# Performance work log

Hardware: AMD Instinct MI355X
Metric: run time of the kernel (lower is better)

The kernel has to match this reference:

```python
import jax, jax.numpy as jnp
import numpy as np

N, E = 50000, 800000
IN_CH, N_HID, OUT_CH = 128, 256, 128
DROPOUT_P = 0.5


def gcn_conv(x, src, dst, ew, W, b, num_nodes):
    # PyG GCNConv with edge_weight: symmetric normalization with self-loops.
    loop = jnp.arange(num_nodes)
    s = jnp.concatenate([src, loop])
    d = jnp.concatenate([dst, loop])
    w = jnp.concatenate([ew, jnp.ones((num_nodes,), ew.dtype)])
    deg = jax.ops.segment_sum(w, d, num_segments=num_nodes)  # [N]
    dinv = jnp.where(deg > 0, jax.lax.rsqrt(deg), 0.0)
    norm = dinv[s] * w * dinv[d]                             # [E+N]
    h = x @ W                                                # [N, out]
    msg = h[s] * norm[:, None]                               # [E+N, out]
    out = jax.ops.segment_sum(msg, d, num_segments=num_nodes)
    return out + b


def setup_inputs() -> dict:
    key = jax.random.key(0)
    ks = jax.random.split(key, 8)
    x = jax.random.normal(ks[0], (N, IN_CH), dtype=jnp.float32)
    edge_index = jax.random.randint(ks[1], (2, E), 0, N, dtype=jnp.int64)
    weight = jax.random.uniform(ks[2], (E,), dtype=jnp.float32)
    # GCNConv params (glorot weights, zero bias)
    s1 = (6.0 / (IN_CH + N_HID)) ** 0.5
    s2 = (6.0 / (N_HID + OUT_CH)) ** 0.5
    W1 = jax.random.uniform(ks[3], (IN_CH, N_HID), jnp.float32, -s1, s1)
    b1 = jnp.zeros((N_HID,), jnp.float32)
    W2 = jax.random.uniform(ks[4], (N_HID, OUT_CH), jnp.float32, -s2, s2)
    b2 = jnp.zeros((OUT_CH,), jnp.float32)
    return {"x": x, "edge_index": edge_index, "weight": weight,
            "W1": W1, "b1": b1, "W2": W2, "b2": b2}


def reference(x, edge_index, weight, W1, b1, W2, b2):
    src, dst = edge_index[0], edge_index[1]
    h = jax.nn.relu(gcn_conv(x, src, dst, weight, W1, b1, N))
    # F.dropout(x, p) with training=True (torch default); fixed key for determinism
    keep = jax.random.bernoulli(jax.random.key(42), 1.0 - DROPOUT_P, h.shape)
    h = jnp.where(keep, h / (1.0 - DROPOUT_P), 0.0)
    return gcn_conv(h, src, dst, weight, W2, b2, N)
```

## Files before the change

kernel.cpp:

```cpp
#include <hip/hip_runtime.h>
#include <hip/hip_bf16.h>
#include <cstdint>

#define INCH 128
#define NHID 256
#define OUTCH 128
#define CAP 64

typedef unsigned short u16;
typedef unsigned long long u64;
typedef __attribute__((ext_vector_type(8))) short s8v;
typedef __attribute__((ext_vector_type(4))) float f4v;

__device__ __forceinline__ u16 tob(float a) {
    unsigned u = __float_as_uint(a);
    return (u16)((u + 0x7fffu + ((u >> 16) & 1u)) >> 16);
}

__device__ __forceinline__ void bsplit(float a, u16& hi, u16& lo) {
    unsigned u = __float_as_uint(a);
    unsigned r = (u + 0x7fffu + ((u >> 16) & 1u)) >> 16;
    hi = (u16)r;
    float res = a - __uint_as_float(r << 16);
    lo = tob(res);
}

__device__ __forceinline__ unsigned rotl32(unsigned x, int d) {
    return (x << d) | (x >> (32 - d));
}

__device__ __forceinline__ void threefry2x32(unsigned k0, unsigned k1,
                                             unsigned x0, unsigned x1,
                                             unsigned& o0, unsigned& o1) {
    unsigned ks2 = k0 ^ k1 ^ 0x1BD11BDAu;
#define TF_R(r) { x0 += x1; x1 = rotl32(x1, (r)); x1 ^= x0; }
    x0 += k0; x1 += k1;
    TF_R(13) TF_R(15) TF_R(26) TF_R(6)
    x0 += k1; x1 += ks2 + 1u;
    TF_R(17) TF_R(29) TF_R(16) TF_R(24)
    x0 += ks2; x1 += k0 + 2u;
    TF_R(13) TF_R(15) TF_R(26) TF_R(6)
    x0 += k0; x1 += k1 + 3u;
    TF_R(17) TF_R(29) TF_R(16) TF_R(24)
    x0 += k1; x1 += ks2 + 4u;
    TF_R(13) TF_R(15) TF_R(26) TF_R(6)
    x0 += ks2; x1 += k0 + 5u;
#undef TF_R
    o0 = x0; o1 = x1;
}

__global__ __launch_bounds__(256) void k_mask(unsigned* __restrict__ mask, int nwords) {
    int i = blockIdx.x * 256 + threadIdx.x;
    if (i >= nwords) return;
    unsigned base = (unsigned)i * 32u;
    unsigned m = 0;
#pragma unroll
    for (int b = 0; b < 32; ++b) {
        unsigned o0, o1;
        threefry2x32(0u, 42u, 0u, base + (unsigned)b, o0, o1);
        m |= ((((o0 ^ o1) >> 31) ^ 1u) & 1u) << b;
    }
    mask[i] = m;
}

__global__ void k_zero(int* cnt, int N) {
    int i = blockIdx.x * blockDim.x + threadIdx.x;
    if (i < N) cnt[i] = 0;
}

__global__ void k_fill(const int* __restrict__ src, const int* __restrict__ dst,
                       const float* __restrict__ w, int* cnt,
                       unsigned* __restrict__ buck, int E) {
    int e = blockIdx.x * blockDim.x + threadIdx.x;
    if (e < E) {
        int d = dst[e];
        int pos = atomicAdd(&cnt[d], 1);
        if (pos < CAP)
            buck[(size_t)d * CAP + pos] = ((unsigned)tob(w[e]) << 16) | (unsigned)src[e];
    }
}

__global__ __launch_bounds__(256) void k_deg(const unsigned* __restrict__ buck,
                                             const int* __restrict__ cnt,
                                             float* __restrict__ dinv, int N) {
    int node = blockIdx.x * 8 + (threadIdx.x >> 5);
    int l = threadIdx.x & 31;
    if (node >= N) return;
    int c = min(cnt[node], CAP);
    float s = 0.f;
    for (int p = l; p < c; p += 32)
        s += __uint_as_float(buck[(size_t)node * CAP + p] & 0xffff0000u);
#pragma unroll
    for (int o = 16; o > 0; o >>= 1) s += __shfl_xor(s, o, 32);
    if (l == 0) dinv[node] = rsqrtf(1.f + s);
}

__global__ __launch_bounds__(256) void k_norm(unsigned* __restrict__ buck,
                                              const int* __restrict__ cnt,
                                              const float* __restrict__ dinv, int N) {
    int node = blockIdx.x * 8 + (threadIdx.x >> 5);
    int l = threadIdx.x & 31;
    if (node >= N) return;
    int c = min(cnt[node], CAP);
    float dd = dinv[node];
    for (int p = l; p < c; p += 32) {
        unsigned u = buck[(size_t)node * CAP + p];
        unsigned s = u & 0xffffu;
        float wv = __uint_as_float(u & 0xffff0000u);
        float v = dinv[s] * wv * dd;
        buck[(size_t)node * CAP + p] = ((unsigned)tob(v) << 16) | s;
    }
}

__global__ void conv_wt(const float* __restrict__ W, u16* __restrict__ Wh,
                        u16* __restrict__ Wl, int K, int N) {
    int i = blockIdx.x * 256 + threadIdx.x;
    if (i >= K * N) return;
    int k = i / N, n = i % N;
    u16 hi, lo;
    bsplit(W[i], hi, lo);
    Wh[(size_t)n * K + k] = hi;
    Wl[(size_t)n * K + k] = lo;
}

__global__ __launch_bounds__(256) void k_tobf16(const float4* __restrict__ in,
                                                uint4* __restrict__ outb, int n8) {
    int i = blockIdx.x * 256 + threadIdx.x;
    if (i >= n8) return;
    float4 a = in[i * 2], b = in[i * 2 + 1];
    uint4 o;
    o.x = (unsigned)tob(a.x) | ((unsigned)tob(a.y) << 16);
    o.y = (unsigned)tob(a.z) | ((unsigned)tob(a.w) << 16);
    o.z = (unsigned)tob(b.x) | ((unsigned)tob(b.y) << 16);
    o.w = (unsigned)tob(b.z) | ((unsigned)tob(b.w) << 16);
    outb[i] = o;
}

template <int BM, int BN, int MODE>
__global__ __launch_bounds__(256) void gemm_mfma(
    const u16* __restrict__ Ah, const u16* __restrict__ Al,
    const u16* __restrict__ Bh, const u16* __restrict__ Bl,
    const float* __restrict__ bias, const unsigned* __restrict__ mask,
    const float* __restrict__ dinv,
    u16* __restrict__ Ch, u16* __restrict__ Cl,
    u16* __restrict__ Cb, float* __restrict__ Sp,
    int M, int Ntot, int K) {
    constexpr int WN = BN / 2;
    constexpr int MFRAG = BM / 32;
    constexpr int NFRAG = WN / 16;
    __shared__ u16 Alh[BM][40], All[BM][40];
    __shared__ u16 Blh[BN][40], Bll[BN][40];

    const int tid = threadIdx.x;
    const int lane = tid & 63;
    const int w = tid >> 6;
    const int wm = (w >> 1) * (BM / 2);
    const int wn = (w & 1) * WN;
    const int l15 = lane & 15;
    const int kh = lane >> 4;
    const int row0 = blockIdx.y * BM;
    const int col0 = blockIdx.x * BN;

    f4v acc[MFRAG][NFRAG];
#pragma unroll
    for (int f = 0; f < MFRAG; ++f)
#pragma unroll
        for (int g = 0; g < NFRAG; ++g) acc[f][g] = (f4v){0.f, 0.f, 0.f, 0.f};

    for (int k0 = 0; k0 < K; k0 += 32) {
#pragma unroll
        for (int c = tid; c < BM * 4; c += 256) {
            int m = c >> 2, ko = (c & 3) * 8;
            int gm = row0 + m;
            uint4 vh = make_uint4(0, 0, 0, 0), vl = make_uint4(0, 0, 0, 0);
            if (gm < M) {
                size_t gi = (size_t)gm * K + k0 + ko;
                vh = *reinterpret_cast<const uint4*>(&Ah[gi]);
                vl = *reinterpret_cast<const uint4*>(&Al[gi]);
            }
            *reinterpret_cast<uint4*>(&Alh[m][ko]) = vh;
            *reinterpret_cast<uint4*>(&All[m][ko]) = vl;
        }
#pragma unroll
        for (int c = tid; c < BN * 4; c += 256) {
            int n = c >> 2, ko = (c & 3) * 8;
            size_t gi = (size_t)(col0 + n) * K + k0 + ko;
            *reinterpret_cast<uint4*>(&Blh[n][ko]) = *reinterpret_cast<const uint4*>(&Bh[gi]);
            *reinterpret_cast<uint4*>(&Bll[n][ko]) = *reinterpret_cast<const uint4*>(&Bl[gi]);
        }
        __syncthreads();

        s8v afh[MFRAG], afl[MFRAG], bfh[NFRAG], bfl[NFRAG];
#pragma unroll
        for (int f = 0; f < MFRAG; ++f) {
            afh[f] = *reinterpret_cast<const s8v*>(&Alh[wm + f * 16 + l15][kh * 8]);
            afl[f] = *reinterpret_cast<const s8v*>(&All[wm + f * 16 + l15][kh * 8]);
        }
#pragma unroll
        for (int g = 0; g < NFRAG; ++g) {
            bfh[g] = *reinterpret_cast<const s8v*>(&Blh[wn + g * 16 + l15][kh * 8]);
            bfl[g] = *reinterpret_cast<const s8v*>(&Bll[wn + g * 16 + l15][kh * 8]);
        }
#pragma unroll
        for (int f = 0; f < MFRAG; ++f)
#pragma unroll
            for (int g = 0; g < NFRAG; ++g) {
                acc[f][g] = __builtin_amdgcn_mfma_f32_16x16x32_bf16(afl[f], bfh[g], acc[f][g], 0, 0, 0);
                acc[f][g] = __builtin_amdgcn_mfma_f32_16x16x32_bf16(afh[f], bfl[g], acc[f][g], 0, 0, 0);
                acc[f][g] = __builtin_amdgcn_mfma_f32_16x16x32_bf16(afh[f], bfh[g], acc[f][g], 0, 0, 0);
            }
        __syncthreads();
    }

#pragma unroll
    for (int f = 0; f < MFRAG; ++f) {
#pragma unroll
        for (int g = 0; g < NFRAG; ++g) {
#pragma unroll
            for (int r = 0; r < 4; ++r) {
                int gr = row0 + wm + f * 16 + kh * 4 + r;
                if (gr >= M) continue;
                int gc = col0 + wn + g * 16 + l15;
                float v = acc[f][g][r];
                if (MODE == 0) {
                    v = fmaxf(v + bias[gc], 0.f);
                    unsigned j = (unsigned)gr * (unsigned)Ntot + (unsigned)gc;
                    unsigned keep = (mask[j >> 5] >> (j & 31u)) & 1u;
                    v = keep ? v * 2.f : 0.f;
                    u16 hi, lo;
                    bsplit(v, hi, lo);
                    Ch[(size_t)gr * Ntot + gc] = hi;
                    Cl[(size_t)gr * Ntot + gc] = lo;
                } else {
                    float d = dinv[gr];
                    Cb[(size_t)gr * Ntot + gc] = tob(v);
                    Sp[(size_t)gr * Ntot + gc] = fmaf(v, d * d, bias[gc]);
                }
            }
        }
    }
}

template <bool SPLIT>
__global__ __launch_bounds__(256) void k_agg_b(const uint4* __restrict__ gb,
                                               const float4* __restrict__ selfs,
                                               const float* __restrict__ dinv,
                                               const int* __restrict__ cnt,
                                               const unsigned* __restrict__ buck,
                                               uint4* __restrict__ outh,
                                               uint4* __restrict__ outl,
                                               float4* __restrict__ outf, int N) {
    int node = blockIdx.x * 16 + (threadIdx.x >> 4);
    int l = threadIdx.x & 15;
    if (node >= N) return;
    float4 s0 = selfs[(size_t)node * 32 + l * 2];
    float4 s1 = selfs[(size_t)node * 32 + l * 2 + 1];
    float a0, a1, a2, a3, a4, a5, a6, a7;
    if (SPLIT) {
        float d = dinv[node], sc = d * d;
        a0 = s0.x * sc; a1 = s0.y * sc; a2 = s0.z * sc; a3 = s0.w * sc;
        a4 = s1.x * sc; a5 = s1.y * sc; a6 = s1.z * sc; a7 = s1.w * sc;
    } else {
        a0 = s0.x; a1 = s0.y; a2 = s0.z; a3 = s0.w;
        a4 = s1.x; a5 = s1.y; a6 = s1.z; a7 = s1.w;
    }
#define ACCB(gv, ev) { float v = __uint_as_float((ev) & 0xffff0000u); \
    a0 = fmaf(__uint_as_float((gv).x << 16), v, a0); \
    a1 = fmaf(__uint_as_float((gv).x & 0xffff0000u), v, a1); \
    a2 = fmaf(__uint_as_float((gv).y << 16), v, a2); \
    a3 = fmaf(__uint_as_float((gv).y & 0xffff0000u), v, a3); \
    a4 = fmaf(__uint_as_float((gv).z << 16), v, a4); \
    a5 = fmaf(__uint_as_float((gv).z & 0xffff0000u), v, a5); \
    a6 = fmaf(__uint_as_float((gv).w << 16), v, a6); \
    a7 = fmaf(__uint_as_float((gv).w & 0xffff0000u), v, a7); }
    int c = min(cnt[node], CAP);
    const unsigned* row = buck + (size_t)node * CAP;
    int p = 0;
    for (; p + 8 <= c; p += 8) {
        unsigned e0 = row[p + 0], e1 = row[p + 1], e2 = row[p + 2], e3 = row[p + 3];
        unsigned e4 = row[p + 4], e5 = row[p + 5], e6 = row[p + 6], e7 = row[p + 7];
        uint4 g0 = gb[(size_t)(e0 & 0xffffu) * 16 + l];
        uint4 g1 = gb[(size_t)(e1 & 0xffffu) * 16 + l];
        uint4 g2 = gb[(size_t)(e2 & 0xffffu) * 16 + l];
        uint4 g3 = gb[(size_t)(e3 & 0xffffu) * 16 + l];
        uint4 g4 = gb[(size_t)(e4 & 0xffffu) * 16 + l];
        uint4 g5 = gb[(size_t)(e5 & 0xffffu) * 16 + l];
        uint4 g6 = gb[(size_t)(e6 & 0xffffu) * 16 + l];
        uint4 g7 = gb[(size_t)(e7 & 0xffffu) * 16 + l];
        ACCB(g0, e0) ACCB(g1, e1) ACCB(g2, e2) ACCB(g3, e3)
        ACCB(g4, e4) ACCB(g5, e5) ACCB(g6, e6) ACCB(g7, e7)
    }
    for (; p < c; ++p) {
        unsigned e = row[p];
        uint4 g = gb[(size_t)(e & 0xffffu) * 16 + l];
        ACCB(g, e)
    }
#undef ACCB
    if (SPLIT) {
        u16 h[8], lo[8];
        bsplit(a0, h[0], lo[0]); bsplit(a1, h[1], lo[1]);
        bsplit(a2, h[2], lo[2]); bsplit(a3, h[3], lo[3]);
        bsplit(a4, h[4], lo[4]); bsplit(a5, h[5], lo[5]);
        bsplit(a6, h[6], lo[6]); bsplit(a7, h[7], lo[7]);
        uint4 oh, ol;
        oh.x = (unsigned)h[0] | ((unsigned)h[1] << 16);
        oh.y = (unsigned)h[2] | ((unsigned)h[3] << 16);
        oh.z = (unsigned)h[4] | ((unsigned)h[5] << 16);
        oh.w = (unsigned)h[6] | ((unsigned)h[7] << 16);
        ol.x = (unsigned)lo[0] | ((unsigned)lo[1] << 16);
        ol.y = (unsigned)lo[2] | ((unsigned)lo[3] << 16);
        ol.z = (unsigned)lo[4] | ((unsigned)lo[5] << 16);
        ol.w = (unsigned)lo[6] | ((unsigned)lo[7] << 16);
        outh[(size_t)node * 16 + l] = oh;
        outl[(size_t)node * 16 + l] = ol;
    } else {
        outf[(size_t)node * 32 + l * 2]     = make_float4(a0, a1, a2, a3);
        outf[(size_t)node * 32 + l * 2 + 1] = make_float4(a4, a5, a6, a7);
    }
}

extern "C" void kernel_launch(void* const* d_in, const int* in_sizes, int n_in,
                              void* d_out, int out_size, void* d_ws, size_t ws_size,
                              hipStream_t stream) {
    (void)n_in; (void)out_size; (void)ws_size;
    const float* x  = (const float*)d_in[0];
    const int*   ei = (const int*)d_in[1];
    const float* w  = (const float*)d_in[2];
    const float* W1 = (const float*)d_in[3];
    const float* b1 = (const float*)d_in[4];
    const float* W2 = (const float*)d_in[5];
    const float* b2 = (const float*)d_in[6];
    float* out = (float*)d_out;

    int N = in_sizes[0] / INCH;
    int E = in_sizes[1] / 2;
    const int* src = ei;
    const int* dst = ei + E;

    char* ws = (char*)d_ws;
    size_t off = 0;
    auto alloc = [&](size_t bytes) -> char* {
        size_t p = (off + 255) & ~(size_t)255;
        off = p + bytes;
        return ws + p;
    };
    int*      cnt    = (int*)     alloc((size_t)N * 4);
    float*    dinv   = (float*)   alloc((size_t)N * 4);
    unsigned* buck   = (unsigned*)alloc((size_t)N * CAP * 4);
    unsigned* mask   = (unsigned*)alloc((size_t)N * NHID / 8);
    u16*      xb     = (u16*)     alloc((size_t)N * INCH * 2);
    u16*      axh    = (u16*)     alloc((size_t)N * INCH * 2);
    u16*      axl    = (u16*)     alloc((size_t)N * INCH * 2);
    u16*      hdh    = (u16*)     alloc((size_t)N * NHID * 2);
    u16*      hdl    = (u16*)     alloc((size_t)N * NHID * 2);
    u16*      w1h    = (u16*)     alloc((size_t)INCH * NHID * 2);
    u16*      w1l    = (u16*)     alloc((size_t)INCH * NHID * 2);
    u16*      w2h    = (u16*)     alloc((size_t)NHID * OUTCH * 2);
    u16*      w2l    = (u16*)     alloc((size_t)NHID * OUTCH * 2);
    u16*      g2b    = xb;
    float*    sp     = (float*)axh;

    int nb = (N + 255) / 256;
    int eb = (E + 255) / 256;
    int nwords = N * NHID / 32;
    int hb = (N + 7) / 8;
    int ab = (N + 15) / 16;

    k_zero<<<nb, 256, 0, stream>>>(cnt, N);
    k_fill<<<eb, 256, 0, stream>>>(src, dst, w, cnt, buck, E);
    k_deg<<<hb, 256, 0, stream>>>(buck, cnt, dinv, N);
    k_norm<<<hb, 256, 0, stream>>>(buck, cnt, dinv, N);
    conv_wt<<<(INCH * NHID + 255) / 256, 256, 0, stream>>>(W1, w1h, w1l, INCH, NHID);
    conv_wt<<<(NHID * OUTCH + 255) / 256, 256, 0, stream>>>(W2, w2h, w2l, NHID, OUTCH);
    k_mask<<<(nwords + 255) / 256, 256, 0, stream>>>(mask, nwords);
    k_tobf16<<<(N * INCH / 8 + 255) / 256, 256, 0, stream>>>((const float4*)x, (uint4*)xb,
                                                             N * INCH / 8);

    k_agg_b<true><<<ab, 256, 0, stream>>>((const uint4*)xb, (const float4*)x, dinv,
                                          cnt, buck, (uint4*)axh, (uint4*)axl,
                                          nullptr, N);
    dim3 gg1(NHID / 128, (N + 63) / 64);
    gemm_mfma<64, 128, 0><<<gg1, 256, 0, stream>>>(axh, axl, w1h, w1l, b1, mask, nullptr,
                                                   hdh, hdl, nullptr, nullptr,
                                                   N, NHID, INCH);
    dim3 gg2(OUTCH / 64, (N + 63) / 64);
    gemm_mfma<64, 64, 1><<<gg2, 256, 0, stream>>>(hdh, hdl, w2h, w2l, b2, nullptr, dinv,
                                                  nullptr, nullptr, g2b, sp,
                                                  N, OUTCH, NHID);
    k_agg_b<false><<<ab, 256, 0, stream>>>((const uint4*)g2b, (const float4*)sp, nullptr,
                                           cnt, buck, nullptr, nullptr,
                                           (float4*)out, N);
}
```

Measured before the change: 315.2 us.

## Fuse degree into fill atomics, merge prep kernels, split aggregation into feature quarters

```diff
diff --git a/kernel.cpp b/kernel.cpp
--- a/kernel.cpp
+++ b/kernel.cpp
@@ -49,59 +49,41 @@
     o0 = x0; o1 = x1;
 }
 
-__global__ __launch_bounds__(256) void k_mask(unsigned* __restrict__ mask, int nwords) {
-    int i = blockIdx.x * 256 + threadIdx.x;
-    if (i >= nwords) return;
-    unsigned base = (unsigned)i * 32u;
-    unsigned m = 0;
-#pragma unroll
-    for (int b = 0; b < 32; ++b) {
-        unsigned o0, o1;
-        threefry2x32(0u, 42u, 0u, base + (unsigned)b, o0, o1);
-        m |= ((((o0 ^ o1) >> 31) ^ 1u) & 1u) << b;
-    }
-    mask[i] = m;
-}
-
-__global__ void k_zero(int* cnt, int N) {
+__global__ void k_zero64(u64* packed, int N) {
     int i = blockIdx.x * blockDim.x + threadIdx.x;
-    if (i < N) cnt[i] = 0;
-}
-
-__global__ void k_fill(const int* __restrict__ src, const int* __restrict__ dst,
-                       const float* __restrict__ w, int* cnt,
-                       unsigned* __restrict__ buck, int E) {
+    if (i < N) packed[i] = 0ull;
+}
+
+__global__ void k_fill64(const int* __restrict__ src, const int* __restrict__ dst,
+                         const float* __restrict__ w, u64* packed,
+                         unsigned* __restrict__ buck, int E) {
     int e = blockIdx.x * blockDim.x + threadIdx.x;
     if (e < E) {
         int d = dst[e];
-        int pos = atomicAdd(&cnt[d], 1);
+        float wv = w[e];
+        u64 a = (1ull << 32) | (u64)__float2uint_rn(wv * 16777216.0f);
+        u64 old = atomicAdd(&packed[d], a);
+        unsigned pos = (unsigned)(old >> 32);
         if (pos < CAP)
-            buck[(size_t)d * CAP + pos] = ((unsigned)tob(w[e]) << 16) | (unsigned)src[e];
-    }
-}
-
-__global__ __launch_bounds__(256) void k_deg(const unsigned* __restrict__ buck,
-                                             const int* __restrict__ cnt,
-                                             float* __restrict__ dinv, int N) {
-    int node = blockIdx.x * 8 + (threadIdx.x >> 5);
-    int l = threadIdx.x & 31;
-    if (node >= N) return;
-    int c = min(cnt[node], CAP);
-    float s = 0.f;
-    for (int p = l; p < c; p += 32)
-        s += __uint_as_float(buck[(size_t)node * CAP + p] & 0xffff0000u);
-#pragma unroll
-    for (int o = 16; o > 0; o >>= 1) s += __shfl_xor(s, o, 32);
-    if (l == 0) dinv[node] = rsqrtf(1.f + s);
+            buck[(size_t)d * CAP + pos] = ((unsigned)tob(wv) << 16) | (unsigned)src[e];
+    }
+}
+
+__global__ void k_dinv(const u64* __restrict__ packed, float* __restrict__ dinv, int N) {
+    int i = blockIdx.x * blockDim.x + threadIdx.x;
+    if (i < N) {
+        float deg = 1.0f + (float)(unsigned)(packed[i] & 0xffffffffull) * (1.0f / 16777216.0f);
+        dinv[i] = rsqrtf(deg);
+    }
 }
 
 __global__ __launch_bounds__(256) void k_norm(unsigned* __restrict__ buck,
-                                              const int* __restrict__ cnt,
+                                              const u64* __restrict__ packed,
                                               const float* __restrict__ dinv, int N) {
     int node = blockIdx.x * 8 + (threadIdx.x >> 5);
     int l = threadIdx.x & 31;
     if (node >= N) return;
-    int c = min(cnt[node], CAP);
+    int c = min((int)(packed[node] >> 32), CAP);
     float dd = dinv[node];
     for (int p = l; p < c; p += 32) {
         unsigned u = buck[(size_t)node * CAP + p];
@@ -112,28 +94,49 @@
     }
 }
 
-__global__ void conv_wt(const float* __restrict__ W, u16* __restrict__ Wh,
-                        u16* __restrict__ Wl, int K, int N) {
+__global__ __launch_bounds__(256) void k_prep(const float4* __restrict__ x,
+                                              uint4* __restrict__ xb,
+                                              unsigned* __restrict__ mask,
+                                              const float* __restrict__ W1,
+                                              u16* __restrict__ w1h, u16* __restrict__ w1l,
+                                              const float* __restrict__ W2,
+                                              u16* __restrict__ w2h, u16* __restrict__ w2l,
+                                              int n8, int nwords) {
     int i = blockIdx.x * 256 + threadIdx.x;
-    if (i >= K * N) return;
-    int k = i / N, n = i % N;
-    u16 hi, lo;
-    bsplit(W[i], hi, lo);
-    Wh[(size_t)n * K + k] = hi;
-    Wl[(size_t)n * K + k] = lo;
-}
-
-__global__ __launch_bounds__(256) void k_tobf16(const float4* __restrict__ in,
-                                                uint4* __restrict__ outb, int n8) {
-    int i = blockIdx.x * 256 + threadIdx.x;
-    if (i >= n8) return;
-    float4 a = in[i * 2], b = in[i * 2 + 1];
-    uint4 o;
-    o.x = (unsigned)tob(a.x) | ((unsigned)tob(a.y) << 16);
-    o.y = (unsigned)tob(a.z) | ((unsigned)tob(a.w) << 16);
-    o.z = (unsigned)tob(b.x) | ((unsigned)tob(b.y) << 16);
-    o.w = (unsigned)tob(b.z) | ((unsigned)tob(b.w) << 16);
-    outb[i] = o;
+    if (i < n8) {
+        float4 a = x[i * 2], b = x[i * 2 + 1];
+        uint4 o;
+        o.x = (unsigned)tob(a.x) | ((unsigned)tob(a.y) << 16);
+        o.y = (unsigned)tob(a.z) | ((unsigned)tob(a.w) << 16);
+        o.z = (unsigned)tob(b.x) | ((unsigned)tob(b.y) << 16);
+        o.w = (unsigned)tob(b.z) | ((unsigned)tob(b.w) << 16);
+        xb[i] = o;
+    }
+    if (i < nwords) {
+        unsigned base = (unsigned)i * 32u;
+        unsigned m = 0;
+#pragma unroll
+        for (int b = 0; b < 32; ++b) {
+            unsigned o0, o1;
+            threefry2x32(0u, 42u, 0u, base + (unsigned)b, o0, o1);
+            m |= ((((o0 ^ o1) >> 31) ^ 1u) & 1u) << b;
+        }
+        mask[i] = m;
+    }
+    if (i < INCH * NHID) {
+        int k = i / NHID, n = i % NHID;
+        u16 hi, lo;
+        bsplit(W1[i], hi, lo);
+        w1h[(size_t)n * INCH + k] = hi;
+        w1l[(size_t)n * INCH + k] = lo;
+    }
+    if (i < NHID * OUTCH) {
+        int k = i / OUTCH, n = i % OUTCH;
+        u16 hi, lo;
+        bsplit(W2[i], hi, lo);
+        w2h[(size_t)n * NHID + k] = hi;
+        w2l[(size_t)n * NHID + k] = lo;
+    }
 }
 
 template <int BM, int BN, int MODE>
@@ -242,19 +245,22 @@
 }
 
 template <bool SPLIT>
-__global__ __launch_bounds__(256) void k_agg_b(const uint4* __restrict__ gb,
+__global__ __launch_bounds__(256) void k_agg_q(const uint4* __restrict__ gb,
                                                const float4* __restrict__ selfs,
                                                const float* __restrict__ dinv,
-                                               const int* __restrict__ cnt,
+                                               const u64* __restrict__ packed,
                                                const unsigned* __restrict__ buck,
                                                uint4* __restrict__ outh,
                                                uint4* __restrict__ outl,
-                                               float4* __restrict__ outf, int N) {
-    int node = blockIdx.x * 16 + (threadIdx.x >> 4);
-    int l = threadIdx.x & 15;
+                                               float4* __restrict__ outf,
+                                               int N, int q) {
+    int node = blockIdx.x * 64 + (threadIdx.x >> 2);
+    int l = threadIdx.x & 3;
     if (node >= N) return;
-    float4 s0 = selfs[(size_t)node * 32 + l * 2];
-    float4 s1 = selfs[(size_t)node * 32 + l * 2 + 1];
+    const int q4 = q * 4 + l;
+    const int q8 = q * 8 + l * 2;
+    float4 s0 = selfs[(size_t)node * 32 + q8];
+    float4 s1 = selfs[(size_t)node * 32 + q8 + 1];
     float a0, a1, a2, a3, a4, a5, a6, a7;
     if (SPLIT) {
         float d = dinv[node], sc = d * d;
@@ -273,26 +279,26 @@
     a5 = fmaf(__uint_as_float((gv).z & 0xffff0000u), v, a5); \
     a6 = fmaf(__uint_as_float((gv).w << 16), v, a6); \
     a7 = fmaf(__uint_as_float((gv).w & 0xffff0000u), v, a7); }
-    int c = min(cnt[node], CAP);
+    int c = min((int)(packed[node] >> 32), CAP);
     const unsigned* row = buck + (size_t)node * CAP;
     int p = 0;
     for (; p + 8 <= c; p += 8) {
         unsigned e0 = row[p + 0], e1 = row[p + 1], e2 = row[p + 2], e3 = row[p + 3];
         unsigned e4 = row[p + 4], e5 = row[p + 5], e6 = row[p + 6], e7 = row[p + 7];
-        uint4 g0 = gb[(size_t)(e0 & 0xffffu) * 16 + l];
-        uint4 g1 = gb[(size_t)(e1 & 0xffffu) * 16 + l];
-        uint4 g2 = gb[(size_t)(e2 & 0xffffu) * 16 + l];
-        uint4 g3 = gb[(size_t)(e3 & 0xffffu) * 16 + l];
-        uint4 g4 = gb[(size_t)(e4 & 0xffffu) * 16 + l];
-        uint4 g5 = gb[(size_t)(e5 & 0xffffu) * 16 + l];
-        uint4 g6 = gb[(size_t)(e6 & 0xffffu) * 16 + l];
-        uint4 g7 = gb[(size_t)(e7 & 0xffffu) * 16 + l];
+        uint4 g0 = gb[(size_t)(e0 & 0xffffu) * 16 + q4];
+        uint4 g1 = gb[(size_t)(e1 & 0xffffu) * 16 + q4];
+        uint4 g2 = gb[(size_t)(e2 & 0xffffu) * 16 + q4];
+        uint4 g3 = gb[(size_t)(e3 & 0xffffu) * 16 + q4];
+        uint4 g4 = gb[(size_t)(e4 & 0xffffu) * 16 + q4];
+        uint4 g5 = gb[(size_t)(e5 & 0xffffu) * 16 + q4];
+        uint4 g6 = gb[(size_t)(e6 & 0xffffu) * 16 + q4];
+        uint4 g7 = gb[(size_t)(e7 & 0xffffu) * 16 + q4];
         ACCB(g0, e0) ACCB(g1, e1) ACCB(g2, e2) ACCB(g3, e3)
         ACCB(g4, e4) ACCB(g5, e5) ACCB(g6, e6) ACCB(g7, e7)
     }
     for (; p < c; ++p) {
         unsigned e = row[p];
-        uint4 g = gb[(size_t)(e & 0xffffu) * 16 + l];
+        uint4 g = gb[(size_t)(e & 0xffffu) * 16 + q4];
         ACCB(g, e)
     }
 #undef ACCB
@@ -311,11 +317,11 @@
         ol.y = (unsigned)lo[2] | ((unsigned)lo[3] << 16);
         ol.z = (unsigned)lo[4] | ((unsigned)lo[5] << 16);
         ol.w = (unsigned)lo[6] | ((unsigned)lo[7] << 16);
-        outh[(size_t)node * 16 + l] = oh;
-        outl[(size_t)node * 16 + l] = ol;
+        outh[(size_t)node * 16 + q4] = oh;
+        outl[(size_t)node * 16 + q4] = ol;
     } else {
-        outf[(size_t)node * 32 + l * 2]     = make_float4(a0, a1, a2, a3);
-        outf[(size_t)node * 32 + l * 2 + 1] = make_float4(a4, a5, a6, a7);
+        outf[(size_t)node * 32 + q8]     = make_float4(a0, a1, a2, a3);
+        outf[(size_t)node * 32 + q8 + 1] = make_float4(a4, a5, a6, a7);
     }
 }
 
@@ -344,7 +350,7 @@
         off = p + bytes;
         return ws + p;
     };
-    int*      cnt    = (int*)     alloc((size_t)N * 4);
+    u64*      packed = (u64*)     alloc((size_t)N * 8);
     float*    dinv   = (float*)   alloc((size_t)N * 4);
     unsigned* buck   = (unsigned*)alloc((size_t)N * CAP * 4);
     unsigned* mask   = (unsigned*)alloc((size_t)N * NHID / 8);
@@ -362,23 +368,22 @@
 
     int nb = (N + 255) / 256;
     int eb = (E + 255) / 256;
+    int n8 = N * INCH / 8;
     int nwords = N * NHID / 32;
     int hb = (N + 7) / 8;
-    int ab = (N + 15) / 16;
-
-    k_zero<<<nb, 256, 0, stream>>>(cnt, N);
-    k_fill<<<eb, 256, 0, stream>>>(src, dst, w, cnt, buck, E);
-    k_deg<<<hb, 256, 0, stream>>>(buck, cnt, dinv, N);
-    k_norm<<<hb, 256, 0, stream>>>(buck, cnt, dinv, N);
-    conv_wt<<<(INCH * NHID + 255) / 256, 256, 0, stream>>>(W1, w1h, w1l, INCH, NHID);
-    conv_wt<<<(NHID * OUTCH + 255) / 256, 256, 0, stream>>>(W2, w2h, w2l, NHID, OUTCH);
-    k_mask<<<(nwords + 255) / 256, 256, 0, stream>>>(mask, nwords);
-    k_tobf16<<<(N * INCH / 8 + 255) / 256, 256, 0, stream>>>((const float4*)x, (uint4*)xb,
-                                                             N * INCH / 8);
-
-    k_agg_b<true><<<ab, 256, 0, stream>>>((const uint4*)xb, (const float4*)x, dinv,
-                                          cnt, buck, (uint4*)axh, (uint4*)axl,
-                                          nullptr, N);
+    int qb = (N + 63) / 64;
+
+    k_zero64<<<nb, 256, 0, stream>>>(packed, N);
+    k_fill64<<<eb, 256, 0, stream>>>(src, dst, w, packed, buck, E);
+    k_dinv<<<nb, 256, 0, stream>>>(packed, dinv, N);
+    k_norm<<<hb, 256, 0, stream>>>(buck, packed, dinv, N);
+    k_prep<<<(n8 + 255) / 256, 256, 0, stream>>>((const float4*)x, (uint4*)xb, mask,
+                                                 W1, w1h, w1l, W2, w2h, w2l, n8, nwords);
+
+    for (int q = 0; q < 4; ++q)
+        k_agg_q<true><<<qb, 256, 0, stream>>>((const uint4*)xb, (const float4*)x, dinv,
+                                              packed, buck, (uint4*)axh, (uint4*)axl,
+                                              nullptr, N, q);
     dim3 gg1(NHID / 128, (N + 63) / 64);
     gemm_mfma<64, 128, 0><<<gg1, 256, 0, stream>>>(axh, axl, w1h, w1l, b1, mask, nullptr,
                                                    hdh, hdl, nullptr, nullptr,
@@ -387,7 +392,8 @@
     gemm_mfma<64, 64, 1><<<gg2, 256, 0, stream>>>(hdh, hdl, w2h, w2l, b2, nullptr, dinv,
                                                   nullptr, nullptr, g2b, sp,
                                                   N, OUTCH, NHID);
-    k_agg_b<false><<<ab, 256, 0, stream>>>((const uint4*)g2b, (const float4*)sp, nullptr,
-                                           cnt, buck, nullptr, nullptr,
-                                           (float4*)out, N);
-}
+    for (int q = 0; q < 4; ++q)
+        k_agg_q<false><<<qb, 256, 0, stream>>>((const uint4*)g2b, (const float4*)sp, nullptr,
+                                               packed, buck, nullptr, nullptr,
+                                               (float4*)out, N, q);
+}
```

Measured after the change: 364.1 us. +15.5%, slower.
